# Kernel optimization log

Measured on AMD Instinct MI355X. Metric: run time of the kernel, lower is better.

The kernel has to match this reference:

```python
import jax, jax.numpy as jnp
import numpy as np

NX = 41                      # cube side: 2*r_max/voxel + 1 with r_max=6.0, voxel=0.3
VOXEL = 0.3
R_MAX = 6.0
MIN_DIST = 0.8
MIN_SEP = max(1, int(round(MIN_DIST / VOXEL)))   # 3 voxels
K = 4                        # topk_per_channel
NEG = -1.0e9                 # fp32 sentinel used by the torch module
VALID_THRESH = -1.0e8


def setup_inputs() -> dict:
    key = jax.random.key(0)
    B, N, C = 1, 128, 4
    G = NX ** 3
    ax = np.arange(NX)
    ii, jj, kk = np.meshgrid(ax, ax, ax, indexing='ij')
    coords = np.stack([ii, jj, kk], axis=-1).reshape(-1, 3)          # [G,3] integer voxel coords
    center = (NX - 1) / 2.0
    grid_xyz = ((coords - center) * VOXEL).astype(np.float32)        # [G,3] local Angstrom coords
    sphere_mask = np.linalg.norm(grid_xyz, axis=-1) <= R_MAX         # [G] bool
    k1, k2, k3 = jax.random.split(key, 3)
    density = jax.random.normal(k1, (B, N, C, G), jnp.float32)
    A = jax.random.normal(k2, (B, N, 3, 3), jnp.float32)
    Rmats, _ = jnp.linalg.qr(A)                                      # proper-ish rotation matrices
    tpos = jax.random.normal(k3, (B, N, 3), jnp.float32)
    node_mask = jnp.ones((B, N), jnp.float32)
    return dict(density=density,
                grid_xyz=jnp.asarray(grid_xyz),
                sphere_mask=jnp.asarray(sphere_mask),
                coords_int=jnp.asarray(coords, jnp.int32),
                Rmats=Rmats, tpos=tpos, node_mask=node_mask)


def extract_peaks(density, grid_xyz, sphere_mask, coords_int):
    # density: [B,N,C,G]; iterative argmax peak-picking with Chebyshev NMS suppression.
    v0 = jnp.where(sphere_mask[None, None, None, :], density, NEG)
    cx = coords_int[:, 0][None, None, None, :]   # [1,1,1,G]
    cy = coords_int[:, 1][None, None, None, :]
    cz = coords_int[:, 2][None, None, None, :]

    def step(v, _):
        idx = jnp.argmax(v, axis=-1)                                   # [B,N,C]
        score = jnp.take_along_axis(v, idx[..., None], axis=-1)[..., 0]
        valid = score > VALID_THRESH
        xyz = grid_xyz[idx]                                            # [B,N,C,3]
        ijk = coords_int[idx]                                          # [B,N,C,3]
        # Chebyshev (max-abs) voxel distance to the picked peak, per axis to avoid a [.,G,3] temp
        d = jnp.maximum(jnp.maximum(jnp.abs(cx - ijk[..., 0:1]),
                                    jnp.abs(cy - ijk[..., 1:2])),
                        jnp.abs(cz - ijk[..., 2:3]))                    # [B,N,C,G]
        suppress = (d <= MIN_SEP) & valid[..., None]
        v = jnp.where(suppress, NEG, v)
        out = (jnp.where(valid, score, NEG),
               jnp.where(valid[..., None], xyz, 0.0),
               valid)
        return v, out

    _, (scores, xyz, mask) = jax.lax.scan(step, v0, None, length=K)
    # K is leading scan axis -> move to axis 3 giving [B,N,C,K,...]
    return (jnp.moveaxis(xyz, 0, 3), jnp.moveaxis(scores, 0, 3), jnp.moveaxis(mask, 0, 3))


def reference(density, grid_xyz, sphere_mask, coords_int, Rmats, tpos, node_mask):
    peaks_xyz, peaks_score, peaks_mask = extract_peaks(density, grid_xyz, sphere_mask, coords_int)
    # local -> global frame: R @ x + t
    coords_global = jnp.einsum('bnij,bnckj->bncki', Rmats, peaks_xyz) + tpos[:, :, None, None, :]
    m = node_mask[..., None, None, None]                                # [B,N,1,1,1]
    coords_local = peaks_xyz * m
    coords_global = coords_global * m
    scores = peaks_score * node_mask[..., None, None]
    mask = peaks_mask & node_mask.astype(bool)[..., None, None]
    return coords_local, coords_global, scores, mask
```

## Files before the change

kernel.cpp:

```cpp
#include <hip/hip_runtime.h>

#define G_VOX  68921
#define GMAX   68920
#define NSEG   272
#define MWORDS 2176
#define NEGV (-1.0e9f)
#define VTH  (-1.0e8f)

__device__ __forceinline__ bool sphere_bit(const float* __restrict__ gxyz, int e) {
    if (e >= G_VOX) return false;
    float gx = gxyz[e * 3 + 0];
    float gy = gxyz[e * 3 + 1];
    float gz = gxyz[e * 3 + 2];
    float s  = __fadd_rn(__fadd_rn(__fmul_rn(gx, gx), __fmul_rn(gy, gy)),
                         __fmul_rn(gz, gz));
    return (__fsqrt_rn(s) <= 6.0f);
}

__global__ __launch_bounds__(256) void build_mask(
    const float* __restrict__ gxyz, unsigned int* __restrict__ mask)
{
    int idx = blockIdx.x * 256 + threadIdx.x;
    unsigned long long bal = __ballot(sphere_bit(gxyz, idx));
    int lane = threadIdx.x & 63;
    if (lane == 0)       mask[idx >> 5] = (unsigned int)bal;
    else if (lane == 32) mask[idx >> 5] = (unsigned int)(bal >> 32);
}

__global__ __launch_bounds__(512) void fused_peaks(
    const float* __restrict__ density,
    const float* __restrict__ gxyz,
    const unsigned int* __restrict__ maskg,
    const float* __restrict__ Rm, const float* __restrict__ tp,
    const float* __restrict__ nmask,
    float* __restrict__ out)
{
    __shared__ unsigned int smask[MWORDS + 2];
    __shared__ float sval[NSEG];
    __shared__ int   sidx[NSEG];
    __shared__ int   flag[NSEG];
    __shared__ int   list[104];
    __shared__ int   nlist;
    __shared__ float rv[8];
    __shared__ int   ri[8];
    __shared__ float pval[4];
    __shared__ int   pidx[4];
    __shared__ int   pki[4], pkj[4], pkk[4];

    const int tid  = threadIdx.x;
    const int nc   = blockIdx.x;
    const int n    = nc >> 2;
    const int h    = (-nc) & 3;
    const int lane = tid & 63;
    const int w    = tid >> 6;
    const float* dens = density + (size_t)nc * G_VOX;

    for (int i = tid; i < MWORDS + 2; i += 512) smask[i] = (i < MWORDS) ? maskg[i] : 0u;
    for (int i = tid; i < NSEG; i += 512) flag[i] = 0;
    __syncthreads();

    for (int j = 0; j < 34; ++j) {
        const int s = w + 8 * j;
        const int e = h + 4 * tid + 2048 * j;
        const int wd = e >> 5, sh = e & 31;
        unsigned long long mw = ((unsigned long long)smask[wd + 1] << 32) | smask[wd];
        const unsigned int bits = (unsigned int)(mw >> sh) & 0xFu;

        float bv = NEGV;
        int   bi = e;
        if (bits) {
            if (e + 3 <= GMAX) {
                float4 d = *reinterpret_cast<const float4*>(dens + e);
                float v0 = (bits & 1u) ? d.x : NEGV;
                float v1 = (bits & 2u) ? d.y : NEGV;
                float v2 = (bits & 4u) ? d.z : NEGV;
                float v3 = (bits & 8u) ? d.w : NEGV;
                if (v0 > bv) { bv = v0; bi = e;     }
                if (v1 > bv) { bv = v1; bi = e + 1; }
                if (v2 > bv) { bv = v2; bi = e + 2; }
                if (v3 > bv) { bv = v3; bi = e + 3; }
            } else {
                #pragma unroll
                for (int u = 0; u < 4; ++u) {
                    if (((bits >> u) & 1u) && e + u <= GMAX) {
                        float v = dens[e + u];
                        if (v > bv) { bv = v; bi = e + u; }
                    }
                }
            }
        }
        #pragma unroll
        for (int off = 32; off > 0; off >>= 1) {
            float ov = __shfl_down(bv, off);
            int   oi = __shfl_down(bi, off);
            if (ov > bv || (ov == bv && oi < bi)) { bv = ov; bi = oi; }
        }
        if (lane == 0) { sval[s] = bv; sidx[s] = bi; }
    }
    __syncthreads();

    for (int p = 0; p < 4; ++p) {
        float bv = -INFINITY;
        int   bi = 0x7FFFFFFF;
        if (tid < NSEG) { bv = sval[tid]; bi = sidx[tid]; }
        #pragma unroll
        for (int off = 32; off > 0; off >>= 1) {
            float ov = __shfl_down(bv, off);
            int   oi = __shfl_down(bi, off);
            if (ov > bv || (ov == bv && oi < bi)) { bv = ov; bi = oi; }
        }
        if (lane == 0) { rv[w] = bv; ri[w] = bi; }
        __syncthreads();
        if (w == 0) {
            bv = (lane < 8) ? rv[lane] : -INFINITY;
            bi = (lane < 8) ? ri[lane] : 0x7FFFFFFF;
            #pragma unroll
            for (int off = 4; off > 0; off >>= 1) {
                float ov = __shfl_down(bv, off);
                int   oi = __shfl_down(bi, off);
                if (ov > bv || (ov == bv && oi < bi)) { bv = ov; bi = oi; }
            }
            if (lane == 0) {
                pval[p] = bv;
                pidx[p] = bi;
                int pi = bi / 1681;
                int rr = bi - pi * 1681;
                int pj = rr / 41;
                pki[p] = pi; pkj[p] = pj; pkk[p] = rr - pj * 41;
                nlist = 0;
            }
        }
        __syncthreads();

        if (p < 3 && pval[p] > VTH) {
            if (tid < 49) {
                int di = tid / 7 - 3, dj = tid % 7 - 3;
                int ii = pki[p] + di, jj = pkj[p] + dj;
                if (ii >= 0 && ii <= 40 && jj >= 0 && jj <= 40) {
                    int k0 = pkk[p] - 3; if (k0 < 0)  k0 = 0;
                    int k1 = pkk[p] + 3; if (k1 > 40) k1 = 40;
                    int b0  = ii * 1681 + jj * 41 + k0;
                    int cnt = k1 - k0 + 1;
                    unsigned long long m = ((1ull << cnt) - 1ull) << (b0 & 31);
                    int w0 = b0 >> 5;
                    atomicAnd(&smask[w0], ~(unsigned int)m);
                    unsigned int hi = (unsigned int)(m >> 32);
                    if (hi) atomicAnd(&smask[w0 + 1], ~hi);
                    int s0 = (b0 > h) ? (b0 - h) >> 8 : 0;
                    int s1 = (b0 + cnt - 1 > h) ? (b0 + cnt - 1 - h) >> 8 : 0;
                    if (atomicMax(&flag[s0], p + 1) < p + 1) {
                        int q = atomicAdd(&nlist, 1); list[q] = s0;
                    }
                    if (s1 != s0 && atomicMax(&flag[s1], p + 1) < p + 1) {
                        int q = atomicAdd(&nlist, 1); list[q] = s1;
                    }
                }
            }
            __syncthreads();
            const int cnt = nlist;
            for (int q = w; q < cnt; q += 8) {
                const int s = list[q];
                const int e = h + 256 * s + 4 * lane;
                const int wd = e >> 5, sh = e & 31;
                unsigned long long mw = ((unsigned long long)smask[wd + 1] << 32) | smask[wd];
                const unsigned int bits = (unsigned int)(mw >> sh) & 0xFu;
                float bv2 = NEGV;
                int   bi2 = e;
                if (bits) {
                    if (e + 3 <= GMAX) {
                        float4 d = *reinterpret_cast<const float4*>(dens + e);
                        float v0 = (bits & 1u) ? d.x : NEGV;
                        float v1 = (bits & 2u) ? d.y : NEGV;
                        float v2 = (bits & 4u) ? d.z : NEGV;
                        float v3 = (bits & 8u) ? d.w : NEGV;
                        if (v0 > bv2) { bv2 = v0; bi2 = e;     }
                        if (v1 > bv2) { bv2 = v1; bi2 = e + 1; }
                        if (v2 > bv2) { bv2 = v2; bi2 = e + 2; }
                        if (v3 > bv2) { bv2 = v3; bi2 = e + 3; }
                    } else {
                        #pragma unroll
                        for (int u = 0; u < 4; ++u) {
                            if (((bits >> u) & 1u) && e + u <= GMAX) {
                                float v = dens[e + u];
                                if (v > bv2) { bv2 = v; bi2 = e + u; }
                            }
                        }
                    }
                }
                #pragma unroll
                for (int off = 32; off > 0; off >>= 1) {
                    float ov = __shfl_down(bv2, off);
                    int   oi = __shfl_down(bi2, off);
                    if (ov > bv2 || (ov == bv2 && oi < bi2)) { bv2 = ov; bi2 = oi; }
                }
                if (lane == 0) { sval[s] = bv2; sidx[s] = bi2; }
            }
        }
        __syncthreads();
    }

    if (tid < 4) {
        const int k   = tid;
        const float val = pval[k];
        const int   idx = pidx[k];
        const bool valid = val > VTH;
        float gx = 0.0f, gy = 0.0f, gz = 0.0f;
        if (valid) {
            gx = gxyz[idx * 3 + 0];
            gy = gxyz[idx * 3 + 1];
            gz = gxyz[idx * 3 + 2];
        }
        const float nm = nmask[n];
        const float* R = Rm + n * 9;
        const float* t = tp + n * 3;
        float wx = R[0] * gx + R[1] * gy + R[2] * gz + t[0];
        float wy = R[3] * gx + R[4] * gy + R[5] * gz + t[1];
        float wz = R[6] * gx + R[7] * gy + R[8] * gz + t[2];

        const size_t o3 = ((size_t)nc * 4 + k) * 3;
        out[o3 + 0] = gx * nm;
        out[o3 + 1] = gy * nm;
        out[o3 + 2] = gz * nm;
        out[6144 + o3 + 0] = wx * nm;
        out[6144 + o3 + 1] = wy * nm;
        out[6144 + o3 + 2] = wz * nm;
        const size_t o1 = (size_t)nc * 4 + k;
        out[12288 + o1] = (valid ? val : NEGV) * nm;
        out[14336 + o1] = (valid && nm != 0.0f) ? 1.0f : 0.0f;
    }
}

extern "C" void kernel_launch(void* const* d_in, const int* in_sizes, int n_in,
                              void* d_out, int out_size, void* d_ws, size_t ws_size,
                              hipStream_t stream) {
    const float* density  = (const float*)d_in[0];
    const float* grid_xyz = (const float*)d_in[1];
    const float* Rm    = (const float*)d_in[4];
    const float* tpos  = (const float*)d_in[5];
    const float* nmask = (const float*)d_in[6];
    float* out = (float*)d_out;

    unsigned int* mask = (unsigned int*)d_ws;

    build_mask<<<dim3(272), dim3(256), 0, stream>>>(grid_xyz, mask);
    fused_peaks<<<dim3(512), dim3(512), 0, stream>>>(density, grid_xyz, mask,
                                                     Rm, tpos, nmask, out);
}
```

Before: 230.9 us.

## Scan segments with 8-lane groups issuing eight float4 loads each

Segment scanning is reorganized so each 8-lane group handles one 256-element segment, issuing eight independent float4 loads per lane before reducing. The reduction shrinks from a 6-step wavefront shuffle to a 3-step xor shuffle. Loads are now unconditional, with out-of-range addresses clamped instead of taking a tail branch. The goal is more memory-level parallelism and fewer shuffles, both in the initial pass and in the rescans after suppression. In exchange it uses more registers, loads masked-out voxels anyway, and with 34 groups over 8 waves the work is uneven (some waves take 5 iterations, others 4).

```diff
diff --git a/kernel.cpp b/kernel.cpp
--- a/kernel.cpp
+++ b/kernel.cpp
@@ -25,6 +25,48 @@
     int lane = threadIdx.x & 63;
     if (lane == 0)       mask[idx >> 5] = (unsigned int)bal;
     else if (lane == 32) mask[idx >> 5] = (unsigned int)(bal >> 32);
+}
+
+__device__ __forceinline__ void seg_scan8(
+    const float* __restrict__ dens, const unsigned int* smask,
+    int s, int h, int l8, int eclamp, float& bv, int& bi)
+{
+    const int ebase = h + 256 * s + 4 * l8;
+    const int sh    = ebase & 31;
+    const int wd0   = ebase >> 5;
+    bv = NEGV; bi = ebase;
+
+    float4       dq[8];
+    unsigned int bq[8];
+    unsigned int wprev = smask[wd0];
+    #pragma unroll
+    for (int q = 0; q < 8; ++q) {
+        const int e = ebase + 32 * q;
+        const unsigned int wnext = smask[wd0 + q + 1];
+        unsigned long long mw = ((unsigned long long)wnext << 32) | wprev;
+        bq[q] = (unsigned int)(mw >> sh) & 0xFu;
+        wprev = wnext;
+        const int ec = (e + 3 <= GMAX) ? e : eclamp;
+        dq[q] = *reinterpret_cast<const float4*>(dens + ec);
+    }
+    #pragma unroll
+    for (int q = 0; q < 8; ++q) {
+        const int e = ebase + 32 * q;
+        float v0 = (bq[q] & 1u) ? dq[q].x : NEGV;
+        float v1 = (bq[q] & 2u) ? dq[q].y : NEGV;
+        float v2 = (bq[q] & 4u) ? dq[q].z : NEGV;
+        float v3 = (bq[q] & 8u) ? dq[q].w : NEGV;
+        if (v0 > bv) { bv = v0; bi = e;     }
+        if (v1 > bv) { bv = v1; bi = e + 1; }
+        if (v2 > bv) { bv = v2; bi = e + 2; }
+        if (v3 > bv) { bv = v3; bi = e + 3; }
+    }
+    #pragma unroll
+    for (int off = 4; off > 0; off >>= 1) {
+        float ov = __shfl_xor(bv, off);
+        int   oi = __shfl_xor(bi, off);
+        if (ov > bv || (ov == bv && oi < bi)) { bv = ov; bi = oi; }
+    }
 }
 
 __global__ __launch_bounds__(512) void fused_peaks(
@@ -53,49 +95,20 @@
     const int h    = (-nc) & 3;
     const int lane = tid & 63;
     const int w    = tid >> 6;
+    const int s8   = lane >> 3;
+    const int l8   = lane & 7;
     const float* dens = density + (size_t)nc * G_VOX;
+    const int eclamp = h + ((GMAX - 3 - h) & ~3);
 
     for (int i = tid; i < MWORDS + 2; i += 512) smask[i] = (i < MWORDS) ? maskg[i] : 0u;
     for (int i = tid; i < NSEG; i += 512) flag[i] = 0;
     __syncthreads();
 
-    for (int j = 0; j < 34; ++j) {
-        const int s = w + 8 * j;
-        const int e = h + 4 * tid + 2048 * j;
-        const int wd = e >> 5, sh = e & 31;
-        unsigned long long mw = ((unsigned long long)smask[wd + 1] << 32) | smask[wd];
-        const unsigned int bits = (unsigned int)(mw >> sh) & 0xFu;
-
-        float bv = NEGV;
-        int   bi = e;
-        if (bits) {
-            if (e + 3 <= GMAX) {
-                float4 d = *reinterpret_cast<const float4*>(dens + e);
-                float v0 = (bits & 1u) ? d.x : NEGV;
-                float v1 = (bits & 2u) ? d.y : NEGV;
-                float v2 = (bits & 4u) ? d.z : NEGV;
-                float v3 = (bits & 8u) ? d.w : NEGV;
-                if (v0 > bv) { bv = v0; bi = e;     }
-                if (v1 > bv) { bv = v1; bi = e + 1; }
-                if (v2 > bv) { bv = v2; bi = e + 2; }
-                if (v3 > bv) { bv = v3; bi = e + 3; }
-            } else {
-                #pragma unroll
-                for (int u = 0; u < 4; ++u) {
-                    if (((bits >> u) & 1u) && e + u <= GMAX) {
-                        float v = dens[e + u];
-                        if (v > bv) { bv = v; bi = e + u; }
-                    }
-                }
-            }
-        }
-        #pragma unroll
-        for (int off = 32; off > 0; off >>= 1) {
-            float ov = __shfl_down(bv, off);
-            int   oi = __shfl_down(bi, off);
-            if (ov > bv || (ov == bv && oi < bi)) { bv = ov; bi = oi; }
-        }
-        if (lane == 0) { sval[s] = bv; sidx[s] = bi; }
+    for (int g = w; g < 34; g += 8) {
+        const int s = g * 8 + s8;
+        float bv; int bi;
+        seg_scan8(dens, smask, s, h, l8, eclamp, bv, bi);
+        if (l8 == 0) { sval[s] = bv; sidx[s] = bi; }
     }
     __syncthreads();
 
@@ -158,42 +171,14 @@
             }
             __syncthreads();
             const int cnt = nlist;
-            for (int q = w; q < cnt; q += 8) {
-                const int s = list[q];
-                const int e = h + 256 * s + 4 * lane;
-                const int wd = e >> 5, sh = e & 31;
-                unsigned long long mw = ((unsigned long long)smask[wd + 1] << 32) | smask[wd];
-                const unsigned int bits = (unsigned int)(mw >> sh) & 0xFu;
-                float bv2 = NEGV;
-                int   bi2 = e;
-                if (bits) {
-                    if (e + 3 <= GMAX) {
-                        float4 d = *reinterpret_cast<const float4*>(dens + e);
-                        float v0 = (bits & 1u) ? d.x : NEGV;
-                        float v1 = (bits & 2u) ? d.y : NEGV;
-                        float v2 = (bits & 4u) ? d.z : NEGV;
-                        float v3 = (bits & 8u) ? d.w : NEGV;
-                        if (v0 > bv2) { bv2 = v0; bi2 = e;     }
-                        if (v1 > bv2) { bv2 = v1; bi2 = e + 1; }
-                        if (v2 > bv2) { bv2 = v2; bi2 = e + 2; }
-                        if (v3 > bv2) { bv2 = v3; bi2 = e + 3; }
-                    } else {
-                        #pragma unroll
-                        for (int u = 0; u < 4; ++u) {
-                            if (((bits >> u) & 1u) && e + u <= GMAX) {
-                                float v = dens[e + u];
-                                if (v > bv2) { bv2 = v; bi2 = e + u; }
-                            }
-                        }
-                    }
+            for (int base = 0; base < cnt; base += 64) {
+                const int slot = base + w * 8 + s8;
+                if (slot < cnt) {
+                    const int s = list[slot];
+                    float bv2; int bi2;
+                    seg_scan8(dens, smask, s, h, l8, eclamp, bv2, bi2);
+                    if (l8 == 0) { sval[s] = bv2; sidx[s] = bi2; }
                 }
-                #pragma unroll
-                for (int off = 32; off > 0; off >>= 1) {
-                    float ov = __shfl_down(bv2, off);
-                    int   oi = __shfl_down(bi2, off);
-                    if (ov > bv2 || (ov == bv2 && oi < bi2)) { bv2 = ov; bi2 = oi; }
-                }
-                if (lane == 0) { sval[s] = bv2; sidx[s] = bi2; }
             }
         }
         __syncthreads();
```

Result: no change. 226.6 us (-1.9%).
